# Kernel optimization log

Measured on AMD Instinct MI355X. Metric: run time of the kernel, lower is better.

## Reference

```python
import jax, jax.numpy as jnp
import numpy as np

N_NODES = 20000   # nodes
IN_DEG = 8        # fixed in-degree -> E = N*D edges, T = E*D triplets
MSG = 64          # message_size


def _build_indices():
    rng = np.random.default_rng(0)
    E = N_NODES * IN_DEG
    # edge e: row[e] -> col[e]; node j's incoming edges are j*D : (j+1)*D
    row = rng.integers(0, N_NODES, size=E).astype(np.int32)          # source j of edge (j->i)
    # triplets of edge e=(j->i): all edges k->j, i.e. incoming edges of row[e]
    idx_kj = (row[:, None] * IN_DEG + np.arange(IN_DEG, dtype=np.int32)[None, :]).reshape(-1)
    idx_ji = np.repeat(np.arange(E, dtype=np.int32), IN_DEG)
    idx_j = np.repeat(row, IN_DEG)   # pooled-to node for each triplet
    return idx_kj, idx_ji, idx_j, E


def setup_inputs() -> dict:
    idx_kj, idx_ji, idx_j, E = _build_indices()
    key = jax.random.key(0)
    ks = jax.random.split(key, 8)
    s1 = 1.0 / np.sqrt(2 * MSG)
    s2 = 1.0 / np.sqrt(MSG)
    return {
        "messages": jax.random.normal(ks[0], (E, MSG), jnp.float32),
        "r": jax.random.normal(ks[1], (E, 2), jnp.float32),
        "W1": jax.random.uniform(ks[2], (2 * MSG, MSG), jnp.float32, -s1, s1),
        "b1": jax.random.uniform(ks[3], (MSG,), jnp.float32, -s1, s1),
        "W2": jax.random.uniform(ks[4], (MSG, MSG), jnp.float32, -s2, s2),
        "b2": jax.random.uniform(ks[5], (MSG,), jnp.float32, -s2, s2),
        "W3": jax.random.uniform(ks[6], (MSG, 1), jnp.float32, -s2, s2),
        "b3": jax.random.uniform(ks[7], (1,), jnp.float32, -s2, s2),
        "idx_kj": jnp.asarray(idx_kj),
        "idx_ji": jnp.asarray(idx_ji),
        "idx_j": jnp.asarray(idx_j),
        "num_nodes": N_NODES,
    }


def reference(messages, r, W1, b1, W2, b2, W3, b3, idx_kj, idx_ji, idx_j, num_nodes):
    # gather triplet messages and run the 3-layer MLP (Linear/Softplus/Linear/Softplus/Linear)
    h = jnp.concatenate([messages[idx_kj], messages[idx_ji]], axis=1)  # [T, 2M]
    h = jax.nn.softplus(h @ W1 + b1)
    h = jax.nn.softplus(h @ W2 + b2)
    m_ijk = h @ W3 + b3                                                # [T, 1]
    # dyad[t,k,j] = r[idx_ji][t,k] * r[idx_kj][t,j]  (einsum 'ij,ik->ikj')
    rk = r[idx_kj]                                                     # [T, 2]
    rj = r[idx_ji]                                                     # [T, 2]
    dyad = (rj[:, :, None] * rk[:, None, :]).reshape(-1, 4)            # [T, 4]
    temp = m_ijk * dyad                                                # [T, 4]
    # global_mean_pool over idx_j
    s = jax.ops.segment_sum(temp, idx_j, num_segments=num_nodes)       # [N, 4]
    cnt = jax.ops.segment_sum(jnp.ones((temp.shape[0],), temp.dtype), idx_j,
                              num_segments=num_nodes)
    out = s / jnp.maximum(cnt, 1.0)[:, None]
    return out.reshape(-1, 2, 2)
```

## Files before the change

kernel.cpp:

```cpp
#include <hip/hip_runtime.h>

typedef _Float16 half8 __attribute__((ext_vector_type(8)));
typedef __fp16 fp16x2 __attribute__((ext_vector_type(2)));
typedef float floatx4 __attribute__((ext_vector_type(4)));

#define MSGW 64
#define DEG 8

__device__ __forceinline__ float softplus_f(float x) {
    float ax = __builtin_fabsf(x);
    float t  = __builtin_amdgcn_exp2f(-1.44269504089f * ax);
    float l  = 0.69314718056f * __builtin_amdgcn_logf(1.0f + t);
    return fmaxf(x, 0.0f) + l;
}

__device__ __forceinline__ half8 cvt8(const float* p) {
    float4 x = *(const float4*)p;
    float4 y = *(const float4*)(p + 4);
    fp16x2 p0 = __builtin_amdgcn_cvt_pkrtz(x.x, x.y);
    fp16x2 p1 = __builtin_amdgcn_cvt_pkrtz(x.z, x.w);
    fp16x2 p2 = __builtin_amdgcn_cvt_pkrtz(y.x, y.y);
    fp16x2 p3 = __builtin_amdgcn_cvt_pkrtz(y.z, y.w);
    half8 h;
    h[0] = (_Float16)p0[0]; h[1] = (_Float16)p0[1];
    h[2] = (_Float16)p1[0]; h[3] = (_Float16)p1[1];
    h[4] = (_Float16)p2[0]; h[5] = (_Float16)p2[1];
    h[6] = (_Float16)p3[0]; h[7] = (_Float16)p3[1];
    return h;
}

__device__ __forceinline__ half8 sp8(half8 z) {
    half8 h;
#pragma unroll
    for (int j = 0; j < 8; j += 2) {
        fp16x2 pk = __builtin_amdgcn_cvt_pkrtz(softplus_f((float)z[j]),
                                               softplus_f((float)z[j + 1]));
        h[j] = (_Float16)pk[0]; h[j + 1] = (_Float16)pk[1];
    }
    return h;
}

__global__ __launch_bounds__(256, 2)
void edge_proj_kernel(const float* __restrict__ messages,
                      const float* __restrict__ W1, const float* __restrict__ b1,
                      _Float16* __restrict__ PQ, int E)
{
    __shared__ _Float16 lw1x[16 * 512];
    __shared__ _Float16 lrep[4][16 * 132];

    const int tid = threadIdx.x;
    for (int i = tid; i < 64 * 128; i += 256) {
        int k = i >> 7, np = i & 127;
        float v = (np < 64) ? W1[k * 64 + np] : W1[(64 + k) * 64 + (np - 64)];
        int ks = k >> 5, qq = (k >> 3) & 3, j = k & 7;
        int nt = np >> 4, sdx = np & 15;
        lw1x[(nt * 2 + ks) * 512 + (qq * 16 + sdx) * 8 + j] = (_Float16)v;
    }
    __syncthreads();

    const int wave = tid >> 6;
    const int lane = tid & 63;
    const int s = lane & 15;
    const int q = lane >> 4;
    const int wtile = blockIdx.x * 4 + wave;
    const int e0 = wtile * 16;
    if (e0 >= E) return;

    float b1v[4];
#pragma unroll
    for (int nt = 0; nt < 4; ++nt) b1v[nt] = b1[nt * 16 + s];

    int er = e0 + s; if (er >= E) er = E - 1;
    const float* mp = messages + (size_t)er * MSGW + q * 8;
    half8 af0 = cvt8(mp);
    half8 af1 = cvt8(mp + 32);

    floatx4 acc[8];
#pragma unroll
    for (int nt = 0; nt < 4; ++nt) { floatx4 z = {0.f, 0.f, 0.f, 0.f}; acc[nt] = z; }
#pragma unroll
    for (int nt = 4; nt < 8; ++nt) {
        float bv = b1v[nt - 4];
        floatx4 iv = {bv, bv, bv, bv};
        acc[nt] = iv;
    }
#pragma unroll
    for (int nt = 0; nt < 8; ++nt) {
        half8 bf0 = *(const half8*)&lw1x[(nt * 2 + 0) * 512 + lane * 8];
        acc[nt] = __builtin_amdgcn_mfma_f32_16x16x32_f16(af0, bf0, acc[nt], 0, 0, 0);
        half8 bf1 = *(const half8*)&lw1x[(nt * 2 + 1) * 512 + lane * 8];
        acc[nt] = __builtin_amdgcn_mfma_f32_16x16x32_f16(af1, bf1, acc[nt], 0, 0, 0);
    }

    _Float16* rep = lrep[wave];
#pragma unroll
    for (int nt = 0; nt < 8; ++nt)
#pragma unroll
        for (int rr = 0; rr < 4; ++rr)
            rep[(q * 4 + rr) * 132 + nt * 16 + s] = (_Float16)acc[nt][rr];
    __asm__ volatile("s_waitcnt lgkmcnt(0)" ::: "memory");

#pragma unroll
    for (int cc = 0; cc < 4; ++cc) {
        int c = cc * 64 + lane;
        int rrow = c >> 4, c16 = c & 15;
        half8 v = *(const half8*)&rep[rrow * 132 + c16 * 8];
        int eg = e0 + rrow;
        if (eg < E)
            *(half8*)&PQ[(size_t)eg * 128 + c16 * 8] = v;
    }
}

__global__ __launch_bounds__(256, 3)
void triplet_mlp2_kernel(const _Float16* __restrict__ PQ,
                         const float* __restrict__ r2,
                         const float* __restrict__ W2, const float* __restrict__ b2,
                         const float* __restrict__ W3, const float* __restrict__ b3,
                         const int* __restrict__ idx_kj,
                         float* __restrict__ sacc, float* __restrict__ cnt,
                         int nChunks)
{
    __shared__ _Float16 lw2x[8 * 512];

    const int tid = threadIdx.x;
    for (int i = tid; i < 64 * 64; i += 256) {
        int k = i >> 6, n = i & 63;
        int ks = k >> 5, qq = (k >> 3) & 3, j = k & 7;
        int nt = n >> 4, sdx = n & 15;
        lw2x[(nt * 2 + ks) * 512 + (qq * 16 + sdx) * 8 + j] = (_Float16)W2[i];
    }
    __syncthreads();

    const int wave = tid >> 6;
    const int lane = tid & 63;
    const int s = lane & 15;
    const int q = lane >> 4;

    half8 w2f[2][4];
#pragma unroll
    for (int nt = 0; nt < 4; ++nt) {
        w2f[0][nt] = *(const half8*)&lw2x[(nt * 2 + 0) * 512 + lane * 8];
        w2f[1][nt] = *(const half8*)&lw2x[(nt * 2 + 1) * 512 + lane * 8];
    }
    float b2v[4], w3v[4];
#pragma unroll
    for (int nt = 0; nt < 4; ++nt) {
        b2v[nt] = b2[nt * 16 + s];
        w3v[nt] = W3[nt * 16 + s];
    }
    const float b3v = b3[0];

    const int T = nChunks * 64;
    const int stride = gridDim.x * 64;

    int t = blockIdx.x * 64 + wave * 16 + s;
    int kj = (t < T) ? idx_kj[t] : 0;

    for (int chunk = blockIdx.x; chunk < nChunks; chunk += gridDim.x) {
        const int t_next = t + stride;
        const int kj_next = idx_kj[(t_next < T) ? t_next : 0];

        const int ji = t >> 3;
        const int jn = kj >> 3;

        const _Float16* pk_ = PQ + (size_t)kj * 128 + q * 8;
        const _Float16* pj_ = PQ + (size_t)ji * 128 + 64 + q * 8;
        half8 z0 = *(const half8*)pk_        + *(const half8*)pj_;
        half8 z1 = *(const half8*)(pk_ + 32) + *(const half8*)(pj_ + 32);
        half8 a20 = sp8(z0);
        half8 a21 = sp8(z1);

        const float rk0 = r2[(size_t)kj * 2];
        const float rk1 = r2[(size_t)kj * 2 + 1];

        floatx4 acc2[4];
#pragma unroll
        for (int nt = 0; nt < 4; ++nt) {
            float bv = b2v[nt];
            floatx4 iv = {bv, bv, bv, bv};
            acc2[nt] = iv;
        }
#pragma unroll
        for (int nt = 0; nt < 4; ++nt) {
            acc2[nt] = __builtin_amdgcn_mfma_f32_16x16x32_f16(a20, w2f[0][nt], acc2[nt], 0, 0, 0);
            acc2[nt] = __builtin_amdgcn_mfma_f32_16x16x32_f16(a21, w2f[1][nt], acc2[nt], 0, 0, 0);
        }

        float part[4];
#pragma unroll
        for (int rr = 0; rr < 4; ++rr) {
            float p = 0.0f;
#pragma unroll
            for (int nt = 0; nt < 4; ++nt)
                p += softplus_f(acc2[nt][rr]) * w3v[nt];
            part[rr] = p;
        }
#pragma unroll
        for (int mask = 1; mask < 16; mask <<= 1)
#pragma unroll
            for (int rr = 0; rr < 4; ++rr)
                part[rr] += __shfl_xor(part[rr], mask, 16);

        const int srcl = (s >> 2) << 4;
        float mr[4];
#pragma unroll
        for (int rr = 0; rr < 4; ++rr)
            mr[rr] = __shfl(part[rr], srcl, 64);
        const int rsel = s & 3;
        float m_mine = mr[0];
        m_mine = (rsel == 1) ? mr[1] : m_mine;
        m_mine = (rsel == 2) ? mr[2] : m_mine;
        m_mine = (rsel == 3) ? mr[3] : m_mine;
        m_mine += b3v;

        float c = m_mine * ((q & 1) ? rk1 : rk0);
        c += __shfl_xor(c, 1, 16);
        c += __shfl_xor(c, 2, 16);
        c += __shfl_xor(c, 4, 16);

        if ((s & 7) == 0) {
            const int aa = q >> 1, bb = q & 1;
            const float rj = r2[(size_t)ji * 2 + aa];
            atomicAdd(&sacc[(size_t)jn * 4 + aa * 2 + bb], rj * c);
            if (q == 0) atomicAdd(&cnt[jn], 8.0f);
        }

        t = t_next;
        kj = kj_next;
    }
}

__global__ __launch_bounds__(256, 3)
void triplet_mlp_fb_kernel(const float* __restrict__ messages,
                           const float* __restrict__ r2,
                           const float* __restrict__ W1, const float* __restrict__ b1,
                           const float* __restrict__ W2, const float* __restrict__ b2,
                           const float* __restrict__ W3, const float* __restrict__ b3,
                           const int* __restrict__ idx_kj,
                           float* __restrict__ sacc, float* __restrict__ cnt,
                           int nChunks)
{
    __shared__ _Float16 lw1x[16 * 512];
    __shared__ _Float16 lw2x[8 * 512];
    __shared__ float lb1[64], lb2[64], lw3[64];
    __shared__ _Float16 lh[4][16 * 72];

    const int tid = threadIdx.x;
    for (int i = tid; i < 128 * 64; i += 256) {
        int k = i >> 6, n = i & 63;
        int ks = k >> 5, q = (k >> 3) & 3, j = k & 7;
        int nt = n >> 4, s = n & 15;
        lw1x[(nt * 4 + ks) * 512 + (q * 16 + s) * 8 + j] = (_Float16)W1[i];
    }
    for (int i = tid; i < 64 * 64; i += 256) {
        int k = i >> 6, n = i & 63;
        int ks = k >> 5, q = (k >> 3) & 3, j = k & 7;
        int nt = n >> 4, s = n & 15;
        lw2x[(nt * 2 + ks) * 512 + (q * 16 + s) * 8 + j] = (_Float16)W2[i];
    }
    if (tid < 64) { lb1[tid] = b1[tid]; lb2[tid] = b2[tid]; lw3[tid] = W3[tid]; }
    __syncthreads();

    const int wave = tid >> 6;
    const int lane = tid & 63;
    const int s = lane & 15;
    const int q = lane >> 4;
    const float b3v = b3[0];
    const int T = nChunks * 64;
    const int stride = gridDim.x * 64;

    _Float16* myh = lh[wave];

    int t = blockIdx.x * 64 + wave * 16 + s;
    int kj = (t < T) ? idx_kj[t] : 0;

    for (int chunk = blockIdx.x; chunk < nChunks; chunk += gridDim.x) {
        const int t_next = t + stride;
        const int kj_next = idx_kj[(t_next < T) ? t_next : 0];

        const int ji = t >> 3;
        const int jn = kj >> 3;

        const float* mk = messages + (size_t)kj * MSGW + q * 8;
        const float* mj = messages + (size_t)ji * MSGW + q * 8;
        half8 afr[4];
        afr[0] = cvt8(mk);
        afr[1] = cvt8(mk + 32);
        afr[2] = cvt8(mj);
        afr[3] = cvt8(mj + 32);

        const float rk0 = r2[(size_t)kj * 2];
        const float rk1 = r2[(size_t)kj * 2 + 1];

        floatx4 acc[4];
#pragma unroll
        for (int nt = 0; nt < 4; ++nt) {
            float bv = lb1[nt * 16 + s];
            floatx4 iv = {bv, bv, bv, bv};
            acc[nt] = iv;
        }
#pragma unroll
        for (int ks = 0; ks < 4; ++ks)
#pragma unroll
            for (int nt = 0; nt < 4; ++nt) {
                half8 bf = *(const half8*)&lw1x[(nt * 4 + ks) * 512 + lane * 8];
                acc[nt] = __builtin_amdgcn_mfma_f32_16x16x32_f16(afr[ks], bf, acc[nt], 0, 0, 0);
            }

#pragma unroll
        for (int nt = 0; nt < 4; ++nt)
#pragma unroll
            for (int rr = 0; rr < 4; ++rr)
                myh[(q * 4 + rr) * 72 + nt * 16 + s] = (_Float16)softplus_f(acc[nt][rr]);
        __asm__ volatile("s_waitcnt lgkmcnt(0)" ::: "memory");

        half8 a2[2];
        a2[0] = *(const half8*)&myh[s * 72 + q * 8];
        a2[1] = *(const half8*)&myh[s * 72 + 32 + q * 8];
        __asm__ volatile("" ::: "memory");

        floatx4 acc2[4];
#pragma unroll
        for (int nt = 0; nt < 4; ++nt) {
            float bv = lb2[nt * 16 + s];
            floatx4 iv = {bv, bv, bv, bv};
            acc2[nt] = iv;
        }
#pragma unroll
        for (int ks = 0; ks < 2; ++ks)
#pragma unroll
            for (int nt = 0; nt < 4; ++nt) {
                half8 bf = *(const half8*)&lw2x[(nt * 2 + ks) * 512 + lane * 8];
                acc2[nt] = __builtin_amdgcn_mfma_f32_16x16x32_f16(a2[ks], bf, acc2[nt], 0, 0, 0);
            }

        float part[4];
#pragma unroll
        for (int rr = 0; rr < 4; ++rr) {
            float p = 0.0f;
#pragma unroll
            for (int nt = 0; nt < 4; ++nt)
                p += softplus_f(acc2[nt][rr]) * lw3[nt * 16 + s];
            part[rr] = p;
        }
#pragma unroll
        for (int mask = 1; mask < 16; mask <<= 1)
#pragma unroll
            for (int rr = 0; rr < 4; ++rr)
                part[rr] += __shfl_xor(part[rr], mask, 16);

        const int srcl = (s >> 2) << 4;
        float mr[4];
#pragma unroll
        for (int rr = 0; rr < 4; ++rr)
            mr[rr] = __shfl(part[rr], srcl, 64);
        const int rsel = s & 3;
        float m_mine = mr[0];
        m_mine = (rsel == 1) ? mr[1] : m_mine;
        m_mine = (rsel == 2) ? mr[2] : m_mine;
        m_mine = (rsel == 3) ? mr[3] : m_mine;
        m_mine += b3v;

        float c = m_mine * ((q & 1) ? rk1 : rk0);
        c += __shfl_xor(c, 1, 16);
        c += __shfl_xor(c, 2, 16);
        c += __shfl_xor(c, 4, 16);

        if ((s & 7) == 0) {
            const int aa = q >> 1, bb = q & 1;
            const float rj = r2[(size_t)ji * 2 + aa];
            atomicAdd(&sacc[(size_t)jn * 4 + aa * 2 + bb], rj * c);
            if (q == 0) atomicAdd(&cnt[jn], 8.0f);
        }

        t = t_next;
        kj = kj_next;
    }
}

__global__ void finalize_kernel(const float* __restrict__ sacc, const float* __restrict__ cnt,
                                float* __restrict__ out, int n4) {
    int i = blockIdx.x * 256 + threadIdx.x;
    if (i < n4) {
        float c = cnt[i >> 2];
        out[i] = sacc[i] / fmaxf(c, 1.0f);
    }
}

extern "C" void kernel_launch(void* const* d_in, const int* in_sizes, int n_in,
                              void* d_out, int out_size, void* d_ws, size_t ws_size,
                              hipStream_t stream) {
    const float* messages = (const float*)d_in[0];
    const float* r2       = (const float*)d_in[1];
    const float* W1       = (const float*)d_in[2];
    const float* b1       = (const float*)d_in[3];
    const float* W2       = (const float*)d_in[4];
    const float* b2       = (const float*)d_in[5];
    const float* W3       = (const float*)d_in[6];
    const float* b3       = (const float*)d_in[7];
    const int* idx_kj     = (const int*)d_in[8];

    const int T = in_sizes[8];
    const int E = T / DEG;
    const int N = out_size / 4;
    float* sacc = (float*)d_ws;
    float* cntp = sacc + (size_t)N * 4;

    (void)hipMemsetAsync(d_ws, 0, (size_t)N * 5 * sizeof(float), stream);

    const int nChunks = T / 64;
    int grid = nChunks < 4096 ? nChunks : 4096;

    const size_t pqOff  = (((size_t)N * 5 * sizeof(float)) + 255) & ~(size_t)255;
    const size_t needWs = pqOff + (size_t)E * 128 * sizeof(_Float16);

    if (ws_size >= needWs) {
        _Float16* PQ = (_Float16*)((char*)d_ws + pqOff);
        const int tiles = (E + 15) / 16;
        const int pblocks = (tiles + 3) / 4;
        edge_proj_kernel<<<pblocks, 256, 0, stream>>>(messages, W1, b1, PQ, E);
        triplet_mlp2_kernel<<<grid, 256, 0, stream>>>(PQ, r2, W2, b2, W3, b3,
                                                      idx_kj, sacc, cntp, nChunks);
    } else {
        triplet_mlp_fb_kernel<<<grid, 256, 0, stream>>>(messages, r2, W1, b1, W2, b2, W3, b3,
                                                        idx_kj, sacc, cntp, nChunks);
    }

    const int n4 = N * 4;
    finalize_kernel<<<(n4 + 255) / 256, 256, 0, stream>>>(sacc, cntp, (float*)d_out, n4);
}
```

Baseline: 190.5 us.

## Pre-swizzle weights once, persist edge-proj blocks, prefetch triplet gathers, DPP reductions

Adds a one-block kernel that converts W1/W2 to fp16 in MFMA fragment order once, so edge_proj copies them straight into LDS and triplet_mlp2 loads its W2 fragments from global memory with no LDS staging or barrier. edge_proj becomes a persistent grid-stride loop capped at 640 blocks, which amortises the per-block weight setup. The triplet kernel software-pipelines the PQ and r gathers one iteration ahead and replaces the shuffle-based reductions with DPP adds plus one ds_bpermute. The trade-offs are an extra kernel launch and higher register pressure from the prefetched fragments.

```diff
diff --git a/kernel.cpp b/kernel.cpp
--- a/kernel.cpp
+++ b/kernel.cpp
@@ -40,97 +40,125 @@
     return h;
 }
 
+template<int CTRL>
+__device__ __forceinline__ float dpp_addf(float x) {
+    int y = __builtin_amdgcn_update_dpp(0, __float_as_int(x), CTRL, 0xF, 0xF, true);
+    return x + __int_as_float(y);
+}
+__device__ __forceinline__ float red16(float x) {
+    x = dpp_addf<0xB1>(x);
+    x = dpp_addf<0x4E>(x);
+    x = dpp_addf<0x141>(x);
+    x = dpp_addf<0x140>(x);
+    return x;
+}
+__device__ __forceinline__ float red8(float x) {
+    x = dpp_addf<0xB1>(x);
+    x = dpp_addf<0x4E>(x);
+    x = dpp_addf<0x141>(x);
+    return x;
+}
+
+__global__ void prep_weights_kernel(const float* __restrict__ W1, const float* __restrict__ W2,
+                                    _Float16* __restrict__ W1f, _Float16* __restrict__ W2f) {
+    const int tid = threadIdx.x;
+    for (int idx = tid; idx < 16 * 512; idx += 256) {
+        int f = idx >> 9, lane = (idx >> 3) & 63, j = idx & 7;
+        int nt = f >> 1, ks = f & 1;
+        int k = ks * 32 + (lane >> 4) * 8 + j;
+        int np = nt * 16 + (lane & 15);
+        float v = (np < 64) ? W1[k * 64 + np] : W1[(64 + k) * 64 + (np - 64)];
+        W1f[idx] = (_Float16)v;
+    }
+    for (int idx = tid; idx < 8 * 512; idx += 256) {
+        int f = idx >> 9, lane = (idx >> 3) & 63, j = idx & 7;
+        int nt = f >> 1, ks = f & 1;
+        int k = ks * 32 + (lane >> 4) * 8 + j;
+        int n = nt * 16 + (lane & 15);
+        W2f[idx] = (_Float16)W2[k * 64 + n];
+    }
+}
+
 __global__ __launch_bounds__(256, 2)
 void edge_proj_kernel(const float* __restrict__ messages,
-                      const float* __restrict__ W1, const float* __restrict__ b1,
-                      _Float16* __restrict__ PQ, int E)
+                      const _Float16* __restrict__ W1f, const float* __restrict__ b1,
+                      _Float16* __restrict__ PQ, int E, int nbt)
 {
-    __shared__ _Float16 lw1x[16 * 512];
-    __shared__ _Float16 lrep[4][16 * 132];
+    __shared__ __align__(16) _Float16 lw1x[16 * 512];
+    __shared__ __align__(16) _Float16 lrep[4][16 * 132];
 
     const int tid = threadIdx.x;
-    for (int i = tid; i < 64 * 128; i += 256) {
-        int k = i >> 7, np = i & 127;
-        float v = (np < 64) ? W1[k * 64 + np] : W1[(64 + k) * 64 + (np - 64)];
-        int ks = k >> 5, qq = (k >> 3) & 3, j = k & 7;
-        int nt = np >> 4, sdx = np & 15;
-        lw1x[(nt * 2 + ks) * 512 + (qq * 16 + sdx) * 8 + j] = (_Float16)v;
-    }
+    for (int i = tid; i < 1024; i += 256)
+        *(half8*)&lw1x[i * 8] = *(const half8*)&W1f[i * 8];
     __syncthreads();
 
     const int wave = tid >> 6;
     const int lane = tid & 63;
     const int s = lane & 15;
     const int q = lane >> 4;
-    const int wtile = blockIdx.x * 4 + wave;
-    const int e0 = wtile * 16;
-    if (e0 >= E) return;
 
     float b1v[4];
 #pragma unroll
     for (int nt = 0; nt < 4; ++nt) b1v[nt] = b1[nt * 16 + s];
 
-    int er = e0 + s; if (er >= E) er = E - 1;
-    const float* mp = messages + (size_t)er * MSGW + q * 8;
-    half8 af0 = cvt8(mp);
-    half8 af1 = cvt8(mp + 32);
-
-    floatx4 acc[8];
-#pragma unroll
-    for (int nt = 0; nt < 4; ++nt) { floatx4 z = {0.f, 0.f, 0.f, 0.f}; acc[nt] = z; }
-#pragma unroll
-    for (int nt = 4; nt < 8; ++nt) {
-        float bv = b1v[nt - 4];
-        floatx4 iv = {bv, bv, bv, bv};
-        acc[nt] = iv;
-    }
-#pragma unroll
-    for (int nt = 0; nt < 8; ++nt) {
-        half8 bf0 = *(const half8*)&lw1x[(nt * 2 + 0) * 512 + lane * 8];
-        acc[nt] = __builtin_amdgcn_mfma_f32_16x16x32_f16(af0, bf0, acc[nt], 0, 0, 0);
-        half8 bf1 = *(const half8*)&lw1x[(nt * 2 + 1) * 512 + lane * 8];
-        acc[nt] = __builtin_amdgcn_mfma_f32_16x16x32_f16(af1, bf1, acc[nt], 0, 0, 0);
-    }
-
     _Float16* rep = lrep[wave];
-#pragma unroll
-    for (int nt = 0; nt < 8; ++nt)
-#pragma unroll
-        for (int rr = 0; rr < 4; ++rr)
-            rep[(q * 4 + rr) * 132 + nt * 16 + s] = (_Float16)acc[nt][rr];
-    __asm__ volatile("s_waitcnt lgkmcnt(0)" ::: "memory");
-
-#pragma unroll
-    for (int cc = 0; cc < 4; ++cc) {
-        int c = cc * 64 + lane;
-        int rrow = c >> 4, c16 = c & 15;
-        half8 v = *(const half8*)&rep[rrow * 132 + c16 * 8];
-        int eg = e0 + rrow;
-        if (eg < E)
-            *(half8*)&PQ[(size_t)eg * 128 + c16 * 8] = v;
+
+    for (int bt = blockIdx.x; bt < nbt; bt += gridDim.x) {
+        const int e0 = (bt * 4 + wave) * 16;
+        if (e0 >= E) continue;
+        int er = e0 + s; if (er >= E) er = E - 1;
+        const float* mp = messages + (size_t)er * MSGW + q * 8;
+        half8 af0 = cvt8(mp);
+        half8 af1 = cvt8(mp + 32);
+
+        floatx4 acc[8];
+#pragma unroll
+        for (int nt = 0; nt < 4; ++nt) { floatx4 z = {0.f, 0.f, 0.f, 0.f}; acc[nt] = z; }
+#pragma unroll
+        for (int nt = 4; nt < 8; ++nt) {
+            float bv = b1v[nt - 4];
+            floatx4 iv = {bv, bv, bv, bv};
+            acc[nt] = iv;
+        }
+#pragma unroll
+        for (int nt = 0; nt < 8; ++nt) {
+            half8 bf0 = *(const half8*)&lw1x[(nt * 2 + 0) * 512 + lane * 8];
+            acc[nt] = __builtin_amdgcn_mfma_f32_16x16x32_f16(af0, bf0, acc[nt], 0, 0, 0);
+            half8 bf1 = *(const half8*)&lw1x[(nt * 2 + 1) * 512 + lane * 8];
+            acc[nt] = __builtin_amdgcn_mfma_f32_16x16x32_f16(af1, bf1, acc[nt], 0, 0, 0);
+        }
+
+#pragma unroll
+        for (int nt = 0; nt < 8; ++nt)
+#pragma unroll
+            for (int rr = 0; rr < 4; ++rr)
+                rep[(q * 4 + rr) * 132 + nt * 16 + s] = (_Float16)acc[nt][rr];
+        __asm__ volatile("s_waitcnt lgkmcnt(0)" ::: "memory");
+
+#pragma unroll
+        for (int cc = 0; cc < 4; ++cc) {
+            int c = cc * 64 + lane;
+            int rrow = c >> 4, c16 = c & 15;
+            half8 v = *(const half8*)&rep[rrow * 132 + c16 * 8];
+            int eg = e0 + rrow;
+            if (eg < E)
+                *(half8*)&PQ[(size_t)eg * 128 + c16 * 8] = v;
+        }
+        __asm__ volatile("" ::: "memory");
     }
 }
 
 __global__ __launch_bounds__(256, 3)
 void triplet_mlp2_kernel(const _Float16* __restrict__ PQ,
                          const float* __restrict__ r2,
-                         const float* __restrict__ W2, const float* __restrict__ b2,
+                         const _Float16* __restrict__ W2f,
+                         const float* __restrict__ b2,
                          const float* __restrict__ W3, const float* __restrict__ b3,
                          const int* __restrict__ idx_kj,
                          float* __restrict__ sacc, float* __restrict__ cnt,
                          int nChunks)
 {
-    __shared__ _Float16 lw2x[8 * 512];
-
     const int tid = threadIdx.x;
-    for (int i = tid; i < 64 * 64; i += 256) {
-        int k = i >> 6, n = i & 63;
-        int ks = k >> 5, qq = (k >> 3) & 3, j = k & 7;
-        int nt = n >> 4, sdx = n & 15;
-        lw2x[(nt * 2 + ks) * 512 + (qq * 16 + sdx) * 8 + j] = (_Float16)W2[i];
-    }
-    __syncthreads();
-
     const int wave = tid >> 6;
     const int lane = tid & 63;
     const int s = lane & 15;
@@ -139,8 +167,8 @@
     half8 w2f[2][4];
 #pragma unroll
     for (int nt = 0; nt < 4; ++nt) {
-        w2f[0][nt] = *(const half8*)&lw2x[(nt * 2 + 0) * 512 + lane * 8];
-        w2f[1][nt] = *(const half8*)&lw2x[(nt * 2 + 1) * 512 + lane * 8];
+        w2f[0][nt] = *(const half8*)&W2f[(nt * 2 + 0) * 512 + lane * 8];
+        w2f[1][nt] = *(const half8*)&W2f[(nt * 2 + 1) * 512 + lane * 8];
     }
     float b2v[4], w3v[4];
 #pragma unroll
@@ -149,29 +177,42 @@
         w3v[nt] = W3[nt * 16 + s];
     }
     const float b3v = b3[0];
+    const int bperm_addr = (((s >> 2) << 4) + s) << 2;
 
     const int T = nChunks * 64;
     const int stride = gridDim.x * 64;
 
     int t = blockIdx.x * 64 + wave * 16 + s;
-    int kj = (t < T) ? idx_kj[t] : 0;
+    int kj = idx_kj[t];
+    int t1 = t + stride; int t1c = (t1 < T) ? t1 : 0;
+    int kjn = idx_kj[t1c];
+
+    const _Float16* pk0 = PQ + (size_t)kj * 128 + q * 8;
+    const _Float16* pj0 = PQ + (size_t)(t >> 3) * 128 + 64 + q * 8;
+    half8 p0 = *(const half8*)pk0;
+    half8 p1 = *(const half8*)(pk0 + 32);
+    half8 q0 = *(const half8*)pj0;
+    half8 q1 = *(const half8*)(pj0 + 32);
+    float2 rkv = *(const float2*)(r2 + (size_t)kj * 2);
 
     for (int chunk = blockIdx.x; chunk < nChunks; chunk += gridDim.x) {
-        const int t_next = t + stride;
-        const int kj_next = idx_kj[(t_next < T) ? t_next : 0];
+        int t2 = t + 2 * stride; int t2c = (t2 < T) ? t2 : 0;
+        const int kj2 = idx_kj[t2c];
+        const _Float16* pkn = PQ + (size_t)kjn * 128 + q * 8;
+        const _Float16* pjn = PQ + (size_t)(t1c >> 3) * 128 + 64 + q * 8;
+        half8 np0 = *(const half8*)pkn;
+        half8 np1 = *(const half8*)(pkn + 32);
+        half8 nq0 = *(const half8*)pjn;
+        half8 nq1 = *(const half8*)(pjn + 32);
+        float2 nrk = *(const float2*)(r2 + (size_t)kjn * 2);
 
         const int ji = t >> 3;
         const int jn = kj >> 3;
 
-        const _Float16* pk_ = PQ + (size_t)kj * 128 + q * 8;
-        const _Float16* pj_ = PQ + (size_t)ji * 128 + 64 + q * 8;
-        half8 z0 = *(const half8*)pk_        + *(const half8*)pj_;
-        half8 z1 = *(const half8*)(pk_ + 32) + *(const half8*)(pj_ + 32);
+        half8 z0 = p0 + q0;
+        half8 z1 = p1 + q1;
         half8 a20 = sp8(z0);
         half8 a21 = sp8(z1);
-
-        const float rk0 = r2[(size_t)kj * 2];
-        const float rk1 = r2[(size_t)kj * 2 + 1];
 
         floatx4 acc2[4];
 #pragma unroll
@@ -193,30 +234,19 @@
 #pragma unroll
             for (int nt = 0; nt < 4; ++nt)
                 p += softplus_f(acc2[nt][rr]) * w3v[nt];
-            part[rr] = p;
-        }
-#pragma unroll
-        for (int mask = 1; mask < 16; mask <<= 1)
-#pragma unroll
-            for (int rr = 0; rr < 4; ++rr)
-                part[rr] += __shfl_xor(part[rr], mask, 16);
-
-        const int srcl = (s >> 2) << 4;
-        float mr[4];
-#pragma unroll
-        for (int rr = 0; rr < 4; ++rr)
-            mr[rr] = __shfl(part[rr], srcl, 64);
+            part[rr] = red16(p);
+        }
+
         const int rsel = s & 3;
-        float m_mine = mr[0];
-        m_mine = (rsel == 1) ? mr[1] : m_mine;
-        m_mine = (rsel == 2) ? mr[2] : m_mine;
-        m_mine = (rsel == 3) ? mr[3] : m_mine;
-        m_mine += b3v;
-
-        float c = m_mine * ((q & 1) ? rk1 : rk0);
-        c += __shfl_xor(c, 1, 16);
-        c += __shfl_xor(c, 2, 16);
-        c += __shfl_xor(c, 4, 16);
+        float mm = part[0];
+        mm = (rsel == 1) ? part[1] : mm;
+        mm = (rsel == 2) ? part[2] : mm;
+        mm = (rsel == 3) ? part[3] : mm;
+        mm = __int_as_float(__builtin_amdgcn_ds_bpermute(bperm_addr, __float_as_int(mm)));
+        mm += b3v;
+
+        float c = mm * ((q & 1) ? rkv.y : rkv.x);
+        c = red8(c);
 
         if ((s & 7) == 0) {
             const int aa = q >> 1, bb = q & 1;
@@ -225,8 +255,11 @@
             if (q == 0) atomicAdd(&cnt[jn], 8.0f);
         }
 
-        t = t_next;
-        kj = kj_next;
+        t += stride;
+        kj = kjn; kjn = kj2;
+        t1c = t2c;
+        p0 = np0; p1 = np1; q0 = nq0; q1 = nq1;
+        rkv = nrk;
     }
 }
 
@@ -412,14 +445,23 @@
     int grid = nChunks < 4096 ? nChunks : 4096;
 
     const size_t pqOff  = (((size_t)N * 5 * sizeof(float)) + 255) & ~(size_t)255;
-    const size_t needWs = pqOff + (size_t)E * 128 * sizeof(_Float16);
+    const size_t w1fOff = pqOff + (size_t)E * 128 * sizeof(_Float16);
+    const size_t w2fOff = w1fOff + (size_t)16 * 512 * sizeof(_Float16);
+    const size_t needWs = w2fOff + (size_t)8 * 512 * sizeof(_Float16);
 
     if (ws_size >= needWs) {
-        _Float16* PQ = (_Float16*)((char*)d_ws + pqOff);
+        _Float16* PQ  = (_Float16*)((char*)d_ws + pqOff);
+        _Float16* W1f = (_Float16*)((char*)d_ws + w1fOff);
+        _Float16* W2f = (_Float16*)((char*)d_ws + w2fOff);
+
+        prep_weights_kernel<<<1, 256, 0, stream>>>(W1, W2, W1f, W2f);
+
         const int tiles = (E + 15) / 16;
-        const int pblocks = (tiles + 3) / 4;
-        edge_proj_kernel<<<pblocks, 256, 0, stream>>>(messages, W1, b1, PQ, E);
-        triplet_mlp2_kernel<<<grid, 256, 0, stream>>>(PQ, r2, W2, b2, W3, b3,
+        const int nbt = (tiles + 3) / 4;
+        const int epgrid = nbt < 640 ? nbt : 640;
+        edge_proj_kernel<<<epgrid, 256, 0, stream>>>(messages, W1f, b1, PQ, E, nbt);
+
+        triplet_mlp2_kernel<<<grid, 256, 0, stream>>>(PQ, r2, W2f, b2, W3, b3,
                                                       idx_kj, sacc, cntp, nChunks);
     } else {
         triplet_mlp_fb_kernel<<<grid, 256, 0, stream>>>(messages, r2, W1, b1, W2, b2, W3, b3,
```

New measurement: 186.8 us. No clear change (-1.9%).
